# Performance work log

Hardware: AMD Instinct MI355X
Metric: run time of the kernel (lower is better)

## Reference

```python
import math
import jax, jax.numpy as jnp
import numpy as np

B, S, D, H = 4, 1024, 1024, 16
HD = D // H
EPS = 1e-5


def _sinusoidal_encodings(length, d):
    pos = jnp.arange(length, dtype=jnp.float32)
    inv_freq = 1.0 / (10000.0 ** (jnp.arange(0.0, d, 2.0) / d))
    angles = pos[:, None] * inv_freq[None, :]  # [L, D/2]
    enc = jnp.zeros((length, d), dtype=jnp.float32)
    enc = enc.at[:, 0::2].set(jnp.sin(angles))
    enc = enc.at[:, 1::2].set(jnp.cos(angles))
    return enc


def _relative_shift(emb):
    # emb: [B, H, L, L] -- Transformer-XL shift trick
    b, h, l1, l2 = emb.shape
    padded = jnp.concatenate([jnp.zeros((b, h, l1, 1), emb.dtype), emb], axis=-1)
    padded = padded.reshape(b, h, l2 + 1, l1)
    return padded[:, :, 1:, :].reshape(b, h, l1, l2)


def setup_inputs() -> dict:
    key = jax.random.key(0)
    ks = jax.random.split(key, 12)
    s = 0.02
    inp = {
        "x": jax.random.normal(ks[0], (B, S, D), dtype=jnp.float32),
        "Wq": jax.random.normal(ks[1], (D, D), dtype=jnp.float32) * s,
        "bq": jnp.zeros((D,), jnp.float32),
        "Wk": jax.random.normal(ks[2], (D, D), dtype=jnp.float32) * s,
        "bk": jnp.zeros((D,), jnp.float32),
        "Wv": jax.random.normal(ks[3], (D, D), dtype=jnp.float32) * s,
        "bv": jnp.zeros((D,), jnp.float32),
        "Wpos": jax.random.normal(ks[4], (D, D), dtype=jnp.float32) * s,
        "Wf": jax.random.normal(ks[5], (D, D), dtype=jnp.float32) * s,
        "bf": jnp.zeros((D,), jnp.float32),
        "u": jax.random.normal(ks[6], (H, HD), dtype=jnp.float32) * s,
        "v": jax.random.normal(ks[7], (H, HD), dtype=jnp.float32) * s,
        "gamma": jnp.ones((D,), jnp.float32),
        "beta": jnp.zeros((D,), jnp.float32),
    }
    return inp


def reference(x, Wq, bq, Wk, bk, Wv, bv, Wpos, Wf, bf, u, v, gamma, beta):
    b, s, d = x.shape
    # LayerNorm
    mu = jnp.mean(x, axis=-1, keepdims=True)
    var = jnp.mean((x - mu) ** 2, axis=-1, keepdims=True)
    xn = (x - mu) * jax.lax.rsqrt(var + EPS) * gamma + beta

    pe = _sinusoidal_encodings(s, d)  # [S, D]

    q = (xn @ Wq + bq).reshape(b, s, H, HD)
    k = (xn @ Wk + bk).reshape(b, s, H, HD)
    val = (xn @ Wv + bv).reshape(b, s, H, HD)
    p = (pe @ Wpos).reshape(s, H, HD)

    # content-content and content-position scores
    AC = jnp.einsum("bihd,bjhd->bhij", q + u, k)
    BD = jnp.einsum("bihd,jhd->bhij", q + v, p)
    BD = _relative_shift(BD)

    attn = jax.nn.softmax((AC + BD) / math.sqrt(d), axis=-1)  # [B,H,S,S]
    out = jnp.einsum("bhij,bjhd->bihd", attn, val).reshape(b, s, d)
    out = out @ Wf + bf  # dropout is identity (p=0 / eval)
    return out
```

## Files before the change

### kernel.cpp

```cpp
#include <hip/hip_runtime.h>
#include <math.h>


typedef __bf16 bf16;
typedef __bf16 bf16x8 __attribute__((ext_vector_type(8)));
typedef __bf16 bf16x4 __attribute__((ext_vector_type(4)));
typedef float f32x4 __attribute__((ext_vector_type(4)));

#define S_ 1024
#define D_ 1024
#define PROWS 3136
#define POFF 1088

#define AS1 __attribute__((address_space(1)))
#define AS3 __attribute__((address_space(3)))

static __device__ __forceinline__ f32x4 mfma16(bf16x8 a, bf16x8 b, f32x4 c) {
  return __builtin_amdgcn_mfma_f32_16x16x32_bf16(a, b, c, 0, 0, 0);
}

static constexpr size_t OXN  = 0;
static constexpr size_t OWTQ = OXN  + (size_t)4096*1024*2;
static constexpr size_t OWTK = OWTQ + (size_t)1024*1024*2;
static constexpr size_t OWTV = OWTK + (size_t)1024*1024*2;
static constexpr size_t OWTP = OWTV + (size_t)1024*1024*2;
static constexpr size_t OWTF = OWTP + (size_t)1024*1024*2;
static constexpr size_t OPE  = OWTF + (size_t)1024*1024*2;
static constexpr size_t OQU  = OPE  + (size_t)1024*1024*2;
static constexpr size_t OQV  = OQU  + (size_t)64*1024*64*2;
static constexpr size_t OKB  = OQV  + (size_t)64*1024*64*2 + 256;
static constexpr size_t OVT  = OKB  + (size_t)64*1024*64*2;
static constexpr size_t OPP  = OVT  + (size_t)64*1024*64*2;
static constexpr size_t PPBYTES = (size_t)16*PROWS*64*2;
static constexpr size_t OOB  = OPP  + PPBYTES;
static constexpr size_t OBU  = OOB  + (size_t)4096*1024*2;
static constexpr size_t OBV2 = OBU  + 4096;

__global__ __launch_bounds__(256) void prep_kernel(
    const float* __restrict__ x, const float* __restrict__ gamma,
    const float* __restrict__ beta, bf16* __restrict__ xn,
    const float* __restrict__ W0, const float* __restrict__ W1,
    const float* __restrict__ W2, const float* __restrict__ W3,
    const float* __restrict__ W4, bf16* __restrict__ outbase,
    const float* __restrict__ bq, const float* __restrict__ u,
    const float* __restrict__ v, float* __restrict__ bu, float* __restrict__ bv2,
    bf16* __restrict__ pe, uint4* __restrict__ pz) {
  int blk = blockIdx.x, t = threadIdx.x;
  __shared__ float tile[32][33];
  __shared__ float red[8];
  if (blk < 4096) {
    int row = blk;
    const float4* xr = (const float4*)(x + (size_t)row * D_);
    float4 vv = xr[t];
    float s  = vv.x + vv.y + vv.z + vv.w;
    float ss = vv.x*vv.x + vv.y*vv.y + vv.z*vv.z + vv.w*vv.w;
    for (int off = 32; off; off >>= 1) {
      s  += __shfl_xor(s, off);
      ss += __shfl_xor(ss, off);
    }
    int wid = t >> 6;
    if ((t & 63) == 0) { red[wid] = s; red[wid + 4] = ss; }
    __syncthreads();
    float S  = red[0] + red[1] + red[2] + red[3];
    float SS = red[4] + red[5] + red[6] + red[7];
    float mu = S * (1.f / 1024.f);
    float rstd = rsqrtf(SS * (1.f / 1024.f) - mu * mu + 1e-5f);
    float4 g  = ((const float4*)gamma)[t];
    float4 bb = ((const float4*)beta)[t];
    bf16x4 o;
    o[0] = (bf16)((vv.x - mu) * rstd * g.x + bb.x);
    o[1] = (bf16)((vv.y - mu) * rstd * g.y + bb.y);
    o[2] = (bf16)((vv.z - mu) * rstd * g.z + bb.z);
    o[3] = (bf16)((vv.w - mu) * rstd * g.w + bb.w);
    *(bf16x4*)(xn + (size_t)row * D_ + t * 4) = o;
  } else if (blk < 9216) {
    int idx = blk - 4096;
    int z = idx >> 10, rem = idx & 1023;
    int bx = rem & 31, by = rem >> 5;
    const float* W = z == 0 ? W0 : z == 1 ? W1 : z == 2 ? W2 : z == 3 ? W3 : W4;
    bf16* WT = outbase + (size_t)z * 1024 * 1024;
    int tx = t & 31, ty = t >> 5;
    #pragma unroll
    for (int i = 0; i < 4; i++)
      tile[ty + i * 8][tx] = W[(size_t)(by * 32 + ty + i * 8) * D_ + bx * 32 + tx];
    __syncthreads();
    #pragma unroll
    for (int i = 0; i < 4; i++)
      WT[(size_t)(bx * 32 + ty + i * 8) * D_ + by * 32 + tx] = (bf16)tile[tx][ty + i * 8];
  } else {
    int mblk = blk - 9216;
    if (mblk < 1024) {
      int pos = mblk;
      #pragma unroll
      for (int pp = 0; pp < 2; pp++) {
        int f = t + pp * 256;
        float inv = expf(-(2.0f * (float)f * (1.0f / 1024.0f)) * 9.210340371976184f);
        float ang = (float)pos * inv;
        pe[(size_t)pos * D_ + 2 * f]     = (bf16)sinf(ang);
        pe[(size_t)pos * D_ + 2 * f + 1] = (bf16)cosf(ang);
      }
    } else if (mblk < 1024 + 1568) {
      int i = (mblk - 1024) * 256 + t;
      pz[i] = make_uint4(0u, 0u, 0u, 0u);
    } else {
      int c = (mblk - 2592) * 256 + t;
      if (c < 1024) { bu[c] = bq[c] + u[c]; bv2[c] = bq[c] + v[c]; }
    }
  }
}

__global__ __launch_bounds__(256) void gemm_qkvp_kernel(
    const bf16* __restrict__ xn, const bf16* __restrict__ pe,
    const bf16* __restrict__ BT,
    const float* __restrict__ bu, const float* __restrict__ bv2,
    const float* __restrict__ bk, const float* __restrict__ bv,
    bf16* __restrict__ quB, bf16* __restrict__ qvB,
    bf16* __restrict__ kbB, bf16* __restrict__ vtB, bf16* __restrict__ ppd) {
  __shared__ __align__(16) bf16 As[128 * 32];
  __shared__ __align__(16) bf16 Bs[128 * 32];
  int lin = blockIdx.x;
  int swz = (lin & 7) * 104 + (lin >> 3);
  int m0, n0, sect;
  const bf16* Abase;
  int nrow0;
  if (swz < 768) {
    int bx = swz % 24, by = swz / 24;
    m0 = by * 128; n0 = bx * 128;
    sect = n0 >> 10;
    Abase = xn; nrow0 = n0;
  } else {
    int pp = swz - 768;
    int bx = pp & 7, by = pp >> 3;
    m0 = by * 128; n0 = bx * 128;
    sect = 3;
    Abase = pe; nrow0 = 3072 + n0;
  }
  int t = threadIdx.x, l = t & 63, w = t >> 6;
  int lr = l & 15, lq = l >> 4;
  int wr = w >> 1, wc = w & 1;
  f32x4 acc[4][4];
  #pragma unroll
  for (int mi = 0; mi < 4; mi++)
    #pragma unroll
    for (int ni = 0; ni < 4; ni++) acc[mi][ni] = (f32x4){0.f, 0.f, 0.f, 0.f};
  int srow = l >> 2, scol = (l & 3) * 8;
  for (int kk = 0; kk < 1024; kk += 32) {
    #pragma unroll
    for (int c2 = 0; c2 < 2; c2++) {
      int ch = w * 2 + c2;
      const bf16* ga = Abase + (size_t)(m0 + ch * 16 + srow) * 1024 + kk + scol;
      __builtin_amdgcn_global_load_lds((const AS1 void*)ga, (AS3 void*)(As + ch * 512), 16, 0, 0);
      const bf16* gb = BT + (size_t)(nrow0 + ch * 16 + srow) * 1024 + kk + scol;
      __builtin_amdgcn_global_load_lds((const AS1 void*)gb, (AS3 void*)(Bs + ch * 512), 16, 0, 0);
    }
    __syncthreads();
    bf16x8 af[4], bfv[4];
    #pragma unroll
    for (int mi = 0; mi < 4; mi++)
      af[mi] = *(const bf16x8*)(As + (wr * 64 + mi * 16 + lr) * 32 + lq * 8);
    #pragma unroll
    for (int ni = 0; ni < 4; ni++)
      bfv[ni] = *(const bf16x8*)(Bs + (wc * 64 + ni * 16 + lr) * 32 + lq * 8);
    if (sect == 2) {
      #pragma unroll
      for (int mi = 0; mi < 4; mi++)
        #pragma unroll
        for (int ni = 0; ni < 4; ni++)
          acc[mi][ni] = mfma16(bfv[ni], af[mi], acc[mi][ni]);
    } else {
      #pragma unroll
      for (int mi = 0; mi < 4; mi++)
        #pragma unroll
        for (int ni = 0; ni < 4; ni++)
          acc[mi][ni] = mfma16(af[mi], bfv[ni], acc[mi][ni]);
    }
    __syncthreads();
  }
  if (sect == 2) {
    #pragma unroll
    for (int mi = 0; mi < 4; mi++)
      #pragma unroll
      for (int ni = 0; ni < 4; ni++)
        #pragma unroll
        for (int rr = 0; rr < 4; rr++) {
          int wcol = (n0 - 2048) + wc * 64 + ni * 16 + lq * 4 + rr;
          int srw  = m0 + wr * 64 + mi * 16 + lr;
          int b = srw >> 10, s = srw & 1023, h = wcol >> 6, hd = wcol & 63;
          vtB[(((size_t)(b * 16 + h)) * 64 + hd) * 1024 + s] =
              (bf16)(acc[mi][ni][rr] + bv[wcol]);
        }
  } else if (sect == 3) {
    #pragma unroll
    for (int mi = 0; mi < 4; mi++)
      #pragma unroll
      for (int ni = 0; ni < 4; ni++)
        #pragma unroll
        for (int rr = 0; rr < 4; rr++) {
          int row = m0 + wr * 64 + mi * 16 + lq * 4 + rr;
          int col = n0 + wc * 64 + ni * 16 + lr;
          int h = col >> 6, hd = col & 63;
          ppd[((size_t)h * PROWS + POFF + row) * 64 + hd] = (bf16)acc[mi][ni][rr];
        }
  } else {
    #pragma unroll
    for (int mi = 0; mi < 4; mi++)
      #pragma unroll
      for (int ni = 0; ni < 4; ni++)
        #pragma unroll
        for (int rr = 0; rr < 4; rr++) {
          int row = m0 + wr * 64 + mi * 16 + lq * 4 + rr;
          int col = n0 + wc * 64 + ni * 16 + lr;
          float vv = acc[mi][ni][rr];
          int b = row >> 10, s = row & 1023;
          if (sect == 0) {
            int h = col >> 6, hd = col & 63;
            size_t idx = (((size_t)(b * 16 + h)) * 1024 + s) * 64 + hd;
            quB[idx] = (bf16)(vv + bu[col]);
            qvB[idx] = (bf16)(vv + bv2[col]);
          } else {
            int c = col - 1024, h = c >> 6, hd = c & 63;
            size_t idx = (((size_t)(b * 16 + h)) * 1024 + s) * 64 + hd;
            kbB[idx] = (bf16)(vv + bk[c]);
          }
        }
  }
}

__global__ __launch_bounds__(256) void gemm_final_kernel(
    const bf16* __restrict__ A, const bf16* __restrict__ BT,
    const float* __restrict__ bias0, float* __restrict__ out0) {
  __shared__ __align__(16) bf16 As[128 * 32];
  __shared__ __align__(16) bf16 Bs[128 * 32];
  int gx = gridDim.x;
  int lin = blockIdx.x + gx * blockIdx.y;
  int cpx = (gx * gridDim.y) >> 3;
  int swz = (lin & 7) * cpx + (lin >> 3);
  int bx = swz % gx, by = swz / gx;
  int m0 = by * 128, n0 = bx * 128;
  int t = threadIdx.x, l = t & 63, w = t >> 6;
  int lr = l & 15, lq = l >> 4;
  int wr = w >> 1, wc = w & 1;
  f32x4 acc[4][4];
  #pragma unroll
  for (int mi = 0; mi < 4; mi++)
    #pragma unroll
    for (int ni = 0; ni < 4; ni++) acc[mi][ni] = (f32x4){0.f, 0.f, 0.f, 0.f};
  int srow = l >> 2, scol = (l & 3) * 8;
  for (int kk = 0; kk < 1024; kk += 32) {
    #pragma unroll
    for (int c2 = 0; c2 < 2; c2++) {
      int ch = w * 2 + c2;
      const bf16* ga = A + (size_t)(m0 + ch * 16 + srow) * 1024 + kk + scol;
      __builtin_amdgcn_global_load_lds((const AS1 void*)ga, (AS3 void*)(As + ch * 512), 16, 0, 0);
      const bf16* gb = BT + (size_t)(n0 + ch * 16 + srow) * 1024 + kk + scol;
      __builtin_amdgcn_global_load_lds((const AS1 void*)gb, (AS3 void*)(Bs + ch * 512), 16, 0, 0);
    }
    __syncthreads();
    bf16x8 af[4], bfv[4];
    #pragma unroll
    for (int mi = 0; mi < 4; mi++)
      af[mi] = *(const bf16x8*)(As + (wr * 64 + mi * 16 + lr) * 32 + lq * 8);
    #pragma unroll
    for (int ni = 0; ni < 4; ni++)
      bfv[ni] = *(const bf16x8*)(Bs + (wc * 64 + ni * 16 + lr) * 32 + lq * 8);
    #pragma unroll
    for (int mi = 0; mi < 4; mi++)
      #pragma unroll
      for (int ni = 0; ni < 4; ni++)
        acc[mi][ni] = mfma16(af[mi], bfv[ni], acc[mi][ni]);
    __syncthreads();
  }
  #pragma unroll
  for (int mi = 0; mi < 4; mi++)
    #pragma unroll
    for (int ni = 0; ni < 4; ni++)
      #pragma unroll
      for (int rr = 0; rr < 4; rr++) {
        int row = m0 + wr * 64 + mi * 16 + lq * 4 + rr;
        int col = n0 + wc * 64 + ni * 16 + lr;
        out0[(size_t)row * 1024 + col] = acc[mi][ni][rr] + bias0[col];
      }
}

__global__ __launch_bounds__(256, 2) void attn_kernel(
    const bf16* __restrict__ qu, const bf16* __restrict__ qv,
    const bf16* __restrict__ kb, const bf16* __restrict__ vt,
    const bf16* __restrict__ ppad, bf16* __restrict__ ob) {
  int bid = blockIdx.x;
  int xcd = bid & 7, slot = bid >> 3;
  int g = slot >> 4, qblk = slot & 15;
  int bh = xcd + 8 * g;
  int h = bh & 15, b = bh >> 4;

  int t = threadIdx.x, l = t & 63, wid = t >> 6;
  int lr = l & 15, lq = l >> 4;
  int w0 = qblk * 64 + wid * 16;
  const bf16* quB = qu + (size_t)bh * S_ * 64;
  const bf16* qvB = qv + (size_t)bh * S_ * 64;
  const char* kBy = (const char*)(kb + (size_t)bh * S_ * 64);
  const char* vBy = (const char*)(vt + (size_t)bh * 64 * S_);
  const bf16* pH  = ppad + (size_t)h * PROWS * 64;

  __shared__ __align__(16) bf16 Kbuf[2][4096];
  __shared__ __align__(16) bf16 Vbuf[2][4096];
  __shared__ __align__(16) bf16 G1s[4][16][84];
  __shared__ __align__(16) bf16 G2s[4][16][84];
  bf16* PlW = &G1s[wid][0][0];

  bf16x8 aqu[2], aqv1[2], aqv2[2];
  #pragma unroll
  for (int ks = 0; ks < 2; ks++) {
    aqu[ks]  = *(const bf16x8*)(quB + (size_t)(w0 + lr) * 64 + ks * 32 + lq * 8);
    aqv1[ks] = *(const bf16x8*)(qvB + (size_t)(w0 + lr) * 64 + ks * 32 + lq * 8);
    aqv2[ks] = *(const bf16x8*)(qvB + (size_t)(w0 + 1 + lr) * 64 + ks * 32 + lq * 8);
  }
  bf16x8 ones;
  #pragma unroll
  for (int e = 0; e < 8; e++) ones[e] = (bf16)1.0f;

  float m_run[4];
  f32x4 accL = (f32x4){0.f, 0.f, 0.f, 0.f};
  f32x4 accO[4];
  #pragma unroll
  for (int rr = 0; rr < 4; rr++) m_run[rr] = -1e30f;
  #pragma unroll
  for (int nf = 0; nf < 4; nf++) accO[nf] = (f32x4){0.f, 0.f, 0.f, 0.f};

  const float SC = 0.045084220f;

  int srow8 = l >> 3;
  int scolb = (l & 7) * 16;
  auto stage = [&](int nb, int j0n) {
    #pragma unroll
    for (int ci = 0; ci < 4; ci++) {
      int c = wid * 4 + ci;
      int cc = c & 7;
      int row = cc * 8 + srow8;
      int colsrc = scolb ^ ((row & 7) << 4);
      if (c < 8) {
        const char* src = kBy + (size_t)(j0n + row) * 128 + colsrc;
        __builtin_amdgcn_global_load_lds((const AS1 void*)src,
            (AS3 void*)(&Kbuf[nb][cc * 512]), 16, 0, 0);
      } else {
        const char* src = vBy + (size_t)row * 2048 + j0n * 2 + colsrc;
        __builtin_amdgcn_global_load_lds((const AS1 void*)src,
            (AS3 void*)(&Vbuf[nb][cc * 512]), 16, 0, 0);
      }
    }
  };

  bf16x8 bpA[10], bpB[10];
  auto loadwin = [&](bf16x8 (&bp)[10], int pb) {
    #pragma unroll
    for (int gf = 0; gf < 5; gf++)
      #pragma unroll
      for (int ks = 0; ks < 2; ks++)
        bp[gf * 2 + ks] = *(const bf16x8*)(pH + (size_t)(pb + gf * 16 + lr) * 64 + ks * 32 + lq * 8);
  };

  stage(0, 0);
  if (w0 >= 63) loadwin(bpA, 1023 - w0 - 15 + POFF);
  __syncthreads();

  auto tile = [&](int tt, bf16x8 (&bpC)[10], bf16x8 (&bpN)[10]) {
    int j0 = tt * 64;
    int cur = tt & 1;
    if (tt < 15) stage(cur ^ 1, j0 + 64);

    const char* Ks = (const char*)&Kbuf[cur][0];
    const char* Vs = (const char*)&Vbuf[cur][0];
    int d = w0 - j0;

    f32x4 accS[4];
    __builtin_amdgcn_s_setprio(1);
    #pragma unroll
    for (int nf = 0; nf < 4; nf++) {
      accS[nf] = (f32x4){0.f, 0.f, 0.f, 0.f};
      int rowk = nf * 16 + lr;
      #pragma unroll
      for (int ks = 0; ks < 2; ks++) {
        int off = ((rowk << 7) + (ks << 6) + (lq << 4)) ^ ((rowk & 7) << 4);
        bf16x8 bk8 = *(const bf16x8*)(Ks + off);
        accS[nf] = mfma16(aqu[ks], bk8, accS[nf]);
      }
    }
    __builtin_amdgcn_s_setprio(0);

    if (d >= 63) {
      #pragma unroll
      for (int gf = 0; gf < 5; gf++) {
        f32x4 gg = (f32x4){0.f, 0.f, 0.f, 0.f};
        gg = mfma16(aqv1[0], bpC[gf * 2 + 0], gg);
        gg = mfma16(aqv1[1], bpC[gf * 2 + 1], gg);
        #pragma unroll
        for (int rr = 0; rr < 4; rr++) G1s[wid][lq * 4 + rr][gf * 16 + lr] = (bf16)gg[rr];
      }
    } else if (d <= -17) {
      #pragma unroll
      for (int gf = 0; gf < 5; gf++) {
        f32x4 gg = (f32x4){0.f, 0.f, 0.f, 0.f};
        gg = mfma16(aqv2[0], bpC[gf * 2 + 0], gg);
        gg = mfma16(aqv2[1], bpC[gf * 2 + 1], gg);
        #pragma unroll
        for (int rr = 0; rr < 4; rr++) G2s[wid][lq * 4 + rr][gf * 16 + lr] = (bf16)gg[rr];
      }
    } else {
      {
        int pb = 1023 - w0 + j0 - 15 + POFF;
        int gmax = (d + 15) >> 4; if (gmax > 4) gmax = 4;
        for (int gf = 0; gf <= gmax; gf++) {
          f32x4 gg = (f32x4){0.f, 0.f, 0.f, 0.f};
          #pragma unroll
          for (int ks = 0; ks < 2; ks++) {
            bf16x8 bp = *(const bf16x8*)(pH + (size_t)(pb + gf * 16 + lr) * 64 + ks * 32 + lq * 8);
            gg = mfma16(aqv1[ks], bp, gg);
          }
          #pragma unroll
          for (int rr = 0; rr < 4; rr++) G1s[wid][lq * 4 + rr][gf * 16 + lr] = (bf16)gg[rr];
        }
      }
      {
        int pb = j0 - w0 - 17 + POFF;
        int t2 = d + 17;
        int gmin = t2 > 0 ? (t2 >> 4) : 0;
        for (int gf = gmin; gf < 5; gf++) {
          f32x4 gg = (f32x4){0.f, 0.f, 0.f, 0.f};
          #pragma unroll
          for (int ks = 0; ks < 2; ks++) {
            bf16x8 bp = *(const bf16x8*)(pH + (size_t)(pb + gf * 16 + lr) * 64 + ks * 32 + lq * 8);
            gg = mfma16(aqv2[ks], bp, gg);
          }
          #pragma unroll
          for (int rr = 0; rr < 4; rr++) G2s[wid][lq * 4 + rr][gf * 16 + lr] = (bf16)gg[rr];
        }
      }
    }

    if (tt < 15) {
      int dn = d - 64;
      int j0n = j0 + 64;
      if (dn >= 63)       loadwin(bpN, 1023 - w0 + j0n - 15 + POFF);
      else if (dn <= -17) loadwin(bpN, j0n - w0 - 17 + POFF);
    }

    float sc[4][4];
    if (d >= 63) {
      #pragma unroll
      for (int nf = 0; nf < 4; nf++)
        #pragma unroll
        for (int rr = 0; rr < 4; rr++) {
          int ii = lq * 4 + rr;
          int u = nf * 16 + lr - ii + 15;
          sc[nf][rr] = (accS[nf][rr] + (float)G1s[wid][ii][u]) * SC;
        }
    } else if (d <= -17) {
      #pragma unroll
      for (int nf = 0; nf < 4; nf++)
        #pragma unroll
        for (int rr = 0; rr < 4; rr++) {
          int ii = lq * 4 + rr;
          int u = nf * 16 + lr - ii + 15;
          sc[nf][rr] = (accS[nf][rr] + (float)G2s[wid][ii][u]) * SC;
        }
    } else {
      #pragma unroll
      for (int nf = 0; nf < 4; nf++)
        #pragma unroll
        for (int rr = 0; rr < 4; rr++) {
          int ii = lq * 4 + rr;
          int jj = nf * 16 + lr;
          int dd = jj - ii;
          int u = dd + 15;
          float g1v = (float)G1s[wid][ii][u];
          float g2v = (float)G2s[wid][ii][u];
          float bd = dd <= d ? g1v : (dd == d + 1 ? 0.f : g2v);
          sc[nf][rr] = (accS[nf][rr] + bd) * SC;
        }
    }

    float lmax[4];
    #pragma unroll
    for (int rr = 0; rr < 4; rr++)
      lmax[rr] = fmaxf(fmaxf(sc[0][rr], sc[1][rr]), fmaxf(sc[2][rr], sc[3][rr]));
    bool ok = (lmax[0] <= m_run[0] + 8.f) && (lmax[1] <= m_run[1] + 8.f) &&
              (lmax[2] <= m_run[2] + 8.f) && (lmax[3] <= m_run[3] + 8.f);
    if (!__all((int)ok)) {
      float rmax[4];
      #pragma unroll
      for (int rr = 0; rr < 4; rr++) rmax[rr] = lmax[rr];
      #pragma unroll
      for (int st = 1; st < 16; st <<= 1)
        #pragma unroll
        for (int rr = 0; rr < 4; rr++) rmax[rr] = fmaxf(rmax[rr], __shfl_xor(rmax[rr], st));
      #pragma unroll
      for (int rr = 0; rr < 4; rr++) {
        float mnew = fmaxf(m_run[rr], rmax[rr]);
        float sv = exp2f(m_run[rr] - mnew);
        m_run[rr] = mnew;
        accL[rr] *= sv;
        #pragma unroll
        for (int nf = 0; nf < 4; nf++) accO[nf][rr] *= sv;
      }
    }

    #pragma unroll
    for (int nf = 0; nf < 4; nf++)
      #pragma unroll
      for (int rr = 0; rr < 4; rr++) {
        float p = exp2f(sc[nf][rr] - m_run[rr]);
        PlW[(lq * 4 + rr) * 72 + nf * 16 + lr] = (bf16)p;
      }

    bf16x8 ap[2];
    #pragma unroll
    for (int ks = 0; ks < 2; ks++)
      ap[ks] = *(const bf16x8*)(PlW + lr * 72 + ks * 32 + lq * 8);
    __builtin_amdgcn_s_setprio(1);
    #pragma unroll
    for (int ks = 0; ks < 2; ks++) accL = mfma16(ap[ks], ones, accL);
    #pragma unroll
    for (int nf = 0; nf < 4; nf++) {
      int rowd = nf * 16 + lr;
      #pragma unroll
      for (int ks = 0; ks < 2; ks++) {
        int off = ((rowd << 7) + (ks << 6) + (lq << 4)) ^ ((rowd & 7) << 4);
        bf16x8 bv8 = *(const bf16x8*)(Vs + off);
        accO[nf] = mfma16(ap[ks], bv8, accO[nf]);
      }
    }
    __builtin_amdgcn_s_setprio(0);

    __syncthreads();
  };

  #pragma unroll 1
  for (int tt = 0; tt < 16; tt += 2) {
    tile(tt,     bpA, bpB);
    tile(tt + 1, bpB, bpA);
  }

  #pragma unroll
  for (int nf = 0; nf < 4; nf++)
    #pragma unroll
    for (int rr = 0; rr < 4; rr++) {
      int i = w0 + lq * 4 + rr;
      float o = accO[nf][rr] / accL[rr];
      ob[((size_t)(b * S_ + i)) * 1024 + h * 64 + nf * 16 + lr] = (bf16)o;
    }
}

extern "C" void kernel_launch(void* const* d_in, const int* in_sizes, int n_in,
                              void* d_out, int out_size, void* d_ws, size_t ws_size,
                              hipStream_t stream) {
  const float* x     = (const float*)d_in[0];
  const float* Wq    = (const float*)d_in[1];
  const float* bq    = (const float*)d_in[2];
  const float* Wk    = (const float*)d_in[3];
  const float* bk    = (const float*)d_in[4];
  const float* Wv    = (const float*)d_in[5];
  const float* bv    = (const float*)d_in[6];
  const float* Wpos  = (const float*)d_in[7];
  const float* Wf    = (const float*)d_in[8];
  const float* bf_   = (const float*)d_in[9];
  const float* u     = (const float*)d_in[10];
  const float* v     = (const float*)d_in[11];
  const float* gamma = (const float*)d_in[12];
  const float* beta  = (const float*)d_in[13];

  char* ws = (char*)d_ws;
  bf16* xn  = (bf16*)(ws + OXN);
  bf16* wtq = (bf16*)(ws + OWTQ);
  bf16* wtf = (bf16*)(ws + OWTF);
  bf16* pe  = (bf16*)(ws + OPE);
  bf16* quB = (bf16*)(ws + OQU);
  bf16* qvB = (bf16*)(ws + OQV);
  bf16* kbB = (bf16*)(ws + OKB);
  bf16* vtB = (bf16*)(ws + OVT);
  bf16* ppd = (bf16*)(ws + OPP);
  bf16* obB = (bf16*)(ws + OOB);
  float* bu  = (float*)(ws + OBU);
  float* bv2 = (float*)(ws + OBV2);

  prep_kernel<<<11812, 256, 0, stream>>>(x, gamma, beta, xn,
                                         Wq, Wk, Wv, Wpos, Wf, wtq,
                                         bq, u, v, bu, bv2, pe, (uint4*)(ws + OPP));

  gemm_qkvp_kernel<<<832, 256, 0, stream>>>(xn, pe, wtq, bu, bv2, bk, bv,
                                            quB, qvB, kbB, vtB, ppd);

  attn_kernel<<<1024, 256, 0, stream>>>(quB, qvB, kbB, vtB, ppd, obB);

  gemm_final_kernel<<<dim3(8, 32), 256, 0, stream>>>(obB, wtf, bf_, (float*)d_out);
}
```

Measured before the change: 235.5 us.

## Transpose positional-score LDS scratch to pack bf16x2 writes and add GEMM occupancy hint

The per-wave G1/G2 scratch buffers holding the position-score tiles are re-laid out transposed, with a row stride of 18 elements. Each lane can now store its four MFMA outputs as two packed bf16x2 writes instead of four scalar 16-bit writes, which should cut LDS store instructions and bank conflicts. Reads in the relative-shift gather are remapped to the new indexing. The QKV/P GEMM kernel also gets a min-blocks-per-CU launch bound of 4, which may restrict register allocation and cause spills.

```diff
diff --git a/kernel.cpp b/kernel.cpp
--- a/kernel.cpp
+++ b/kernel.cpp
@@ -5,6 +5,7 @@
 typedef __bf16 bf16;
 typedef __bf16 bf16x8 __attribute__((ext_vector_type(8)));
 typedef __bf16 bf16x4 __attribute__((ext_vector_type(4)));
+typedef __bf16 bf16x2 __attribute__((ext_vector_type(2)));
 typedef float f32x4 __attribute__((ext_vector_type(4)));
 
 #define S_ 1024
@@ -109,7 +110,7 @@
   }
 }
 
-__global__ __launch_bounds__(256) void gemm_qkvp_kernel(
+__global__ __launch_bounds__(256, 4) void gemm_qkvp_kernel(
     const bf16* __restrict__ xn, const bf16* __restrict__ pe,
     const bf16* __restrict__ BT,
     const float* __restrict__ bu, const float* __restrict__ bv2,
@@ -303,9 +304,11 @@
 
   __shared__ __align__(16) bf16 Kbuf[2][4096];
   __shared__ __align__(16) bf16 Vbuf[2][4096];
-  __shared__ __align__(16) bf16 G1s[4][16][84];
-  __shared__ __align__(16) bf16 G2s[4][16][84];
-  bf16* PlW = &G1s[wid][0][0];
+  __shared__ __align__(16) bf16 Gt1[4][1440];
+  __shared__ __align__(16) bf16 Gt2[4][1440];
+  bf16* G1w = &Gt1[wid][0];
+  bf16* G2w = &Gt2[wid][0];
+  bf16* PlW = G1w;
 
   bf16x8 aqu[2], aqv1[2], aqv2[2];
   #pragma unroll
@@ -362,6 +365,15 @@
   if (w0 >= 63) loadwin(bpA, 1023 - w0 - 15 + POFF);
   __syncthreads();
 
+  auto gwrite = [&](bf16* Gw, int gf, const f32x4& gg) {
+    bf16x2 p0, p1;
+    p0[0] = (bf16)gg[0]; p0[1] = (bf16)gg[1];
+    p1[0] = (bf16)gg[2]; p1[1] = (bf16)gg[3];
+    int base = (gf * 16 + lr) * 18 + lq * 4;
+    *(bf16x2*)(&Gw[base])     = p0;
+    *(bf16x2*)(&Gw[base + 2]) = p1;
+  };
+
   auto tile = [&](int tt, bf16x8 (&bpC)[10], bf16x8 (&bpN)[10]) {
     int j0 = tt * 64;
     int cur = tt & 1;
@@ -392,8 +404,7 @@
         f32x4 gg = (f32x4){0.f, 0.f, 0.f, 0.f};
         gg = mfma16(aqv1[0], bpC[gf * 2 + 0], gg);
         gg = mfma16(aqv1[1], bpC[gf * 2 + 1], gg);
-        #pragma unroll
-        for (int rr = 0; rr < 4; rr++) G1s[wid][lq * 4 + rr][gf * 16 + lr] = (bf16)gg[rr];
+        gwrite(G1w, gf, gg);
       }
     } else if (d <= -17) {
       #pragma unroll
@@ -401,8 +412,7 @@
         f32x4 gg = (f32x4){0.f, 0.f, 0.f, 0.f};
         gg = mfma16(aqv2[0], bpC[gf * 2 + 0], gg);
         gg = mfma16(aqv2[1], bpC[gf * 2 + 1], gg);
-        #pragma unroll
-        for (int rr = 0; rr < 4; rr++) G2s[wid][lq * 4 + rr][gf * 16 + lr] = (bf16)gg[rr];
+        gwrite(G2w, gf, gg);
       }
     } else {
       {
@@ -415,8 +425,7 @@
             bf16x8 bp = *(const bf16x8*)(pH + (size_t)(pb + gf * 16 + lr) * 64 + ks * 32 + lq * 8);
             gg = mfma16(aqv1[ks], bp, gg);
           }
-          #pragma unroll
-          for (int rr = 0; rr < 4; rr++) G1s[wid][lq * 4 + rr][gf * 16 + lr] = (bf16)gg[rr];
+          gwrite(G1w, gf, gg);
         }
       }
       {
@@ -430,8 +439,7 @@
             bf16x8 bp = *(const bf16x8*)(pH + (size_t)(pb + gf * 16 + lr) * 64 + ks * 32 + lq * 8);
             gg = mfma16(aqv2[ks], bp, gg);
           }
-          #pragma unroll
-          for (int rr = 0; rr < 4; rr++) G2s[wid][lq * 4 + rr][gf * 16 + lr] = (bf16)gg[rr];
+          gwrite(G2w, gf, gg);
         }
       }
     }
@@ -451,7 +459,7 @@
         for (int rr = 0; rr < 4; rr++) {
           int ii = lq * 4 + rr;
           int u = nf * 16 + lr - ii + 15;
-          sc[nf][rr] = (accS[nf][rr] + (float)G1s[wid][ii][u]) * SC;
+          sc[nf][rr] = (accS[nf][rr] + (float)G1w[u * 18 + ii]) * SC;
         }
     } else if (d <= -17) {
       #pragma unroll
@@ -460,7 +468,7 @@
         for (int rr = 0; rr < 4; rr++) {
           int ii = lq * 4 + rr;
           int u = nf * 16 + lr - ii + 15;
-          sc[nf][rr] = (accS[nf][rr] + (float)G2s[wid][ii][u]) * SC;
+          sc[nf][rr] = (accS[nf][rr] + (float)G2w[u * 18 + ii]) * SC;
         }
     } else {
       #pragma unroll
@@ -471,8 +479,8 @@
           int jj = nf * 16 + lr;
           int dd = jj - ii;
           int u = dd + 15;
-          float g1v = (float)G1s[wid][ii][u];
-          float g2v = (float)G2s[wid][ii][u];
+          float g1v = (float)G1w[u * 18 + ii];
+          float g2v = (float)G2w[u * 18 + ii];
           float bd = dd <= d ? g1v : (dd == d + 1 ? 0.f : g2v);
           sc[nf][rr] = (accS[nf][rr] + bd) * SC;
         }
```

Result: slower. 534.6 us (+127.1%).
